# Optimization experiments

Measured on AMD Instinct MI355X. Metric: run time of the kernel, lower is better.

The kernel has to match this reference:

```python
import jax, jax.numpy as jnp
import numpy as np

DIM = 1024
NUM_HEADS = 16
HEAD_DIM = DIM // NUM_HEADS
SCALE = HEAD_DIM ** -0.5


def rotate_half(x):
    x1, x2 = jnp.split(x, 2, axis=-1)
    return jnp.concatenate((-x2, x1), axis=-1)


def setup_inputs() -> dict:
    key = jax.random.key(0)
    ks = jax.random.split(key, 8)
    B, N = 2, 2048
    x = jax.random.normal(ks[0], (B, N, DIM), dtype=jnp.float32)
    # RoPE tables, broadcast over batch and heads
    pos = jnp.arange(N, dtype=jnp.float32)[:, None]
    inv_freq = 1.0 / (10000.0 ** (jnp.arange(0, HEAD_DIM, 2, dtype=jnp.float32) / HEAD_DIM))
    ang = pos * inv_freq[None, :]                       # [N, HEAD_DIM/2]
    ang = jnp.concatenate([ang, ang], axis=-1)          # [N, HEAD_DIM]
    rope_cos = jnp.cos(ang)[None, None]                 # [1,1,N,HEAD_DIM]
    rope_sin = jnp.sin(ang)[None, None]
    s = DIM ** -0.5
    qkv_w = jax.random.normal(ks[1], (3 * DIM, DIM), dtype=jnp.float32) * s
    qkv_b = jnp.zeros((3 * DIM,), dtype=jnp.float32)
    proj_w = jax.random.normal(ks[2], (DIM, DIM), dtype=jnp.float32) * s
    proj_b = jnp.zeros((DIM,), dtype=jnp.float32)
    return {"x": x, "rope_cos": rope_cos, "rope_sin": rope_sin,
            "qkv_w": qkv_w, "qkv_b": qkv_b, "proj_w": proj_w, "proj_b": proj_b}


def reference(x, rope_cos, rope_sin, qkv_w, qkv_b, proj_w, proj_b):
    B, N, C = x.shape
    H, D = NUM_HEADS, HEAD_DIM
    qkv = x @ qkv_w.T + qkv_b                            # [B,N,3C]
    qkv = qkv.reshape(B, N, 3, H, D).transpose(2, 0, 3, 1, 4)  # [3,B,H,N,D]
    q, k, v = qkv[0], qkv[1], qkv[2]
    # RoPE on q, k
    q = q * rope_cos + rotate_half(q) * rope_sin
    k = k * rope_cos + rotate_half(k) * rope_sin
    # scaled dot-product attention
    scores = jnp.einsum('bhnd,bhmd->bhnm', q, k) * SCALE
    attn = jax.nn.softmax(scores, axis=-1)
    out = jnp.einsum('bhnm,bhmd->bhnd', attn, v)         # [B,H,N,D]
    out = out.transpose(0, 2, 1, 3).reshape(B, N, C)
    return out @ proj_w.T + proj_b
```

## Files before the change

kernel.cpp:

```cpp
#include <hip/hip_runtime.h>
#include <hip/hip_bf16.h>

#define NUM_HEADS 16
#define HEAD_DIM 64
#define DIM 1024
#define NTOK 2048
#define MTOT 4096

typedef __attribute__((ext_vector_type(8))) short bf16x8;
typedef __attribute__((ext_vector_type(4))) float f32x4;

__device__ __forceinline__ unsigned short f2bf(float f) {
    union { __hip_bfloat16 h; unsigned short u; } c;
    c.h = __float2bfloat16(f);
    return c.u;
}

__device__ __forceinline__ void gload16(const unsigned short* g, unsigned short* l) {
    __builtin_amdgcn_global_load_lds(
        (const __attribute__((address_space(1))) void*)g,
        (__attribute__((address_space(3))) void*)l, 16, 0, 0);
}

__global__ __launch_bounds__(256) void k_conv3(
    const float* __restrict__ s0, unsigned short* __restrict__ d0, int n0,
    const float* __restrict__ s1, unsigned short* __restrict__ d1, int n1,
    const float* __restrict__ s2, unsigned short* __restrict__ d2, int n2)
{
    int blk = blockIdx.x;
    int b0 = n0 >> 11, b1 = n1 >> 11;
    const float* s; unsigned short* d; int i;
    if (blk < b0)            { s = s0; d = d0; i = blk; }
    else if (blk < b0 + b1)  { s = s1; d = d1; i = blk - b0; }
    else                     { s = s2; d = d2; i = blk - b0 - b1; }
    int idx = (i * 256 + threadIdx.x) * 8;
    float4 a = *(const float4*)(s + idx);
    float4 b = *(const float4*)(s + idx + 4);
    union { unsigned short us[8]; uint4 u4; } p;
    p.us[0] = f2bf(a.x); p.us[1] = f2bf(a.y); p.us[2] = f2bf(a.z); p.us[3] = f2bf(a.w);
    p.us[4] = f2bf(b.x); p.us[5] = f2bf(b.y); p.us[6] = f2bf(b.z); p.us[7] = f2bf(b.w);
    *(uint4*)(d + idx) = p.u4;
}

__global__ __launch_bounds__(256) void k_gemm_qkv(
    const unsigned short* __restrict__ xb, const unsigned short* __restrict__ wb,
    const float* __restrict__ bias, const float* __restrict__ rcos,
    const float* __restrict__ rsin,
    unsigned short* __restrict__ qb, unsigned short* __restrict__ kb,
    unsigned short* __restrict__ vtb)
{
    __shared__ __align__(16) unsigned char smem[34816];
    unsigned short* As = (unsigned short*)smem;
    unsigned short* Bs = (unsigned short*)(smem + 16384);

    const int tid  = threadIdx.x;
    const int lane = tid & 63;
    const int wid  = tid >> 6;
    const int lr   = lane & 15;
    const int g    = lane >> 4;
    const int wm   = (wid >> 1) * 64;
    const int wn   = (wid & 1) * 64;
    const int m0   = blockIdx.x * 128;
    const int n0   = blockIdx.y * 128;

    f32x4 acc[4][4];
    #pragma unroll
    for (int i = 0; i < 4; ++i)
        #pragma unroll
        for (int j = 0; j < 4; ++j) acc[i][j] = (f32x4){0.f, 0.f, 0.f, 0.f};

    for (int k0 = 0; k0 < DIM; k0 += 64) {
        #pragma unroll
        for (int it = 0; it < 4; ++it) {
            int p   = tid + it * 256;
            int row = p >> 3;
            int c   = (p & 7) ^ (row & 7);
            gload16(xb + (size_t)(m0 + row) * DIM + k0 + c*8, As + p*8);
            gload16(wb + (size_t)(n0 + row) * DIM + k0 + c*8, Bs + p*8);
        }
        __syncthreads();
        #pragma unroll
        for (int kk = 0; kk < 2; ++kk) {
            bf16x8 af[4], bfr[4];
            #pragma unroll
            for (int i = 0; i < 4; ++i) {
                int row = wm + i*16 + lr;
                af[i] = *(const bf16x8*)(As + row*64 + (((kk*4 + g) ^ (row & 7)) << 3));
            }
            #pragma unroll
            for (int j = 0; j < 4; ++j) {
                int row = wn + j*16 + lr;
                bfr[j] = *(const bf16x8*)(Bs + row*64 + (((kk*4 + g) ^ (row & 7)) << 3));
            }
            #pragma unroll
            for (int i = 0; i < 4; ++i)
                #pragma unroll
                for (int j = 0; j < 4; ++j)
                    acc[i][j] = __builtin_amdgcn_mfma_f32_16x16x32_bf16(af[i], bfr[j], acc[i][j], 0, 0, 0);
        }
        __syncthreads();
    }

    const int sect = n0 >> 10;
    float bq[4];
    #pragma unroll
    for (int j = 0; j < 4; ++j) bq[j] = bias[n0 + wn + j*16 + lr];

    if (sect < 2) {
        unsigned short* dst = sect ? kb : qb;
        const float sc = sect ? 1.0f : 0.125f * 1.44269504088896f;
        const int h = ((n0 & 1023) + wn) >> 6;
        #pragma unroll
        for (int i = 0; i < 4; ++i) {
            #pragma unroll
            for (int v = 0; v < 4; ++v) {
                int gm = m0 + wm + i*16 + g*4 + v;
                int b  = gm >> 11, n = gm & 2047;
                size_t base = ((size_t)(b*NUM_HEADS + h) * NTOK + n) << 6;
                #pragma unroll
                for (int j = 0; j < 4; ++j) {
                    int d = j*16 + lr;
                    float val = acc[i][j][v] + bq[j];
                    float vp  = acc[i][j^2][v] + bq[j^2];
                    float rot = (j < 2) ? -vp : vp;
                    float c = rcos[n*64 + d], s = rsin[n*64 + d];
                    dst[base + d] = f2bf((val * c + rot * s) * sc);
                }
            }
        }
    } else {
        unsigned short (*vt)[136] = (unsigned short (*)[136])smem;
        __syncthreads();
        #pragma unroll
        for (int i = 0; i < 4; ++i)
            #pragma unroll
            for (int j = 0; j < 4; ++j)
                #pragma unroll
                for (int v = 0; v < 4; ++v) {
                    int row = wm + i*16 + g*4 + v;
                    int c   = wn + j*16 + lr;
                    vt[c][row] = f2bf(acc[i][j][v] + bq[j]);
                }
        __syncthreads();
        const int b = m0 >> 11;
        const int nbase = m0 & 2047;
        #pragma unroll
        for (int it = 0; it < 8; ++it) {
            int c   = (tid >> 4) + it * 16;
            int sc2 = (n0 & 1023) + c;
            int hh  = sc2 >> 6, d = sc2 & 63;
            int nloc = (tid & 15) * 8;
            uint4 val = *(uint4*)&vt[c][nloc];
            *(uint4*)(vtb + ((size_t)(b*NUM_HEADS + hh) * HEAD_DIM + d) * NTOK + nbase + nloc) = val;
        }
    }
}

__global__ __launch_bounds__(256, 4) void k_attn(
    const unsigned short* __restrict__ qb, const unsigned short* __restrict__ kb,
    const unsigned short* __restrict__ vtb, unsigned short* __restrict__ attnb)
{
    __shared__ __align__(16) char sb[40960];

    const int tid  = threadIdx.x;
    const int lane = tid & 63;
    const int w    = tid >> 6;
    const int g    = lane >> 4;
    const int lr   = lane & 15;
    const int q0   = blockIdx.x * 64;
    const int bh   = blockIdx.y;
    const int b    = bh >> 4, h = bh & 15;

    int kfoff[2][4], vfoff[2][4], paoff[2], pwoff[4][4];
    #pragma unroll
    for (int kk = 0; kk < 2; ++kk) {
        #pragma unroll
        for (int fn = 0; fn < 4; ++fn) {
            int row = fn*16 + lr;
            int sw  = ((kk*4 + g) ^ (row & 7)) << 4;
            kfoff[kk][fn] = row*128 + sw;
            vfoff[kk][fn] = 16384 + row*128 + sw;
        }
        paoff[kk] = 32768 + w*2048 + lr*128 + (((kk*4 + g) ^ (lr & 7)) << 4);
    }
    #pragma unroll
    for (int fn = 0; fn < 4; ++fn)
        #pragma unroll
        for (int v = 0; v < 4; ++v) {
            int row = g*4 + v, col = fn*16 + lr;
            pwoff[fn][v] = 32768 + w*2048 + row*128 + (((col >> 3) ^ (row & 7)) << 4) + (col & 7)*2;
        }

    const unsigned short* gk[2];
    const unsigned short* gv[2];
    char* dk[2]; char* dv[2];
    {
        const unsigned short* kbase = kb  + (size_t)bh * NTOK * 64;
        const unsigned short* vbase = vtb + (size_t)bh * HEAD_DIM * NTOK;
        #pragma unroll
        for (int hp = 0; hp < 2; ++hp) {
            int p   = tid + hp * 256;
            int row = p >> 3;
            int c   = (p & 7) ^ (row & 7);
            gk[hp] = kbase + row*64 + c*8;
            gv[hp] = vbase + (size_t)row*NTOK + c*8;
            dk[hp] = sb + p*16;
            dv[hp] = sb + 16384 + p*16;
        }
    }

    bf16x8 qa[2];
    {
        size_t qrow = ((size_t)bh * NTOK + q0 + w*16 + lr) * 64;
        #pragma unroll
        for (int kk = 0; kk < 2; ++kk)
            qa[kk] = *(const bf16x8*)(qb + qrow + kk*32 + g*8);
    }

    f32x4 o[4];
    float m_[4], lsum[4];
    #pragma unroll
    for (int fd = 0; fd < 4; ++fd) o[fd] = (f32x4){0.f, 0.f, 0.f, 0.f};
    #pragma unroll
    for (int v = 0; v < 4; ++v) { m_[v] = -1e30f; lsum[v] = 0.f; }

    #pragma unroll
    for (int hp = 0; hp < 2; ++hp) {
        gload16(gk[hp], (unsigned short*)dk[hp]);
        gload16(gv[hp], (unsigned short*)dv[hp]);
        gk[hp] += 4096; gv[hp] += 64;
    }
    __syncthreads();

#define ATTN_ITER(X, DO_STAGE)                                                   \
    {                                                                            \
        if (DO_STAGE) {                                                          \
            _Pragma("unroll")                                                    \
            for (int hp = 0; hp < 2; ++hp) {                                     \
                gload16(gk[hp], (unsigned short*)(dk[hp] + ((X) ^ 8192)));       \
                gload16(gv[hp], (unsigned short*)(dv[hp] + ((X) ^ 8192)));       \
                gk[hp] += 4096; gv[hp] += 64;                                    \
            }                                                                    \
        }                                                                        \
        f32x4 s_[4];                                                             \
        _Pragma("unroll")                                                        \
        for (int fn = 0; fn < 4; ++fn) s_[fn] = (f32x4){0.f, 0.f, 0.f, 0.f};     \
        _Pragma("unroll")                                                        \
        for (int kk = 0; kk < 2; ++kk) {                                         \
            bf16x8 kf[4];                                                        \
            _Pragma("unroll")                                                    \
            for (int fn = 0; fn < 4; ++fn)                                       \
                kf[fn] = *(const bf16x8*)(sb + kfoff[kk][fn] + (X));             \
            __builtin_amdgcn_s_setprio(1);                                       \
            _Pragma("unroll")                                                    \
            for (int fn = 0; fn < 4; ++fn)                                       \
                s_[fn] = __builtin_amdgcn_mfma_f32_16x16x32_bf16(qa[kk], kf[fn], s_[fn], 0, 0, 0); \
            __builtin_amdgcn_s_setprio(0);                                       \
        }                                                                        \
        float lmax[4]; int need = 0;                                             \
        _Pragma("unroll")                                                        \
        for (int v = 0; v < 4; ++v) {                                            \
            lmax[v] = fmaxf(fmaxf(fmaxf(s_[0][v], s_[1][v]), s_[2][v]), s_[3][v]); \
            need |= (lmax[v] > m_[v] + 8.f);                                     \
        }                                                                        \
        if (__any(need)) {                                                       \
            _Pragma("unroll")                                                    \
            for (int v = 0; v < 4; ++v) {                                        \
                float mx = lmax[v];                                              \
                mx = fmaxf(mx, __shfl_xor(mx, 1));                               \
                mx = fmaxf(mx, __shfl_xor(mx, 2));                               \
                mx = fmaxf(mx, __shfl_xor(mx, 4));                               \
                mx = fmaxf(mx, __shfl_xor(mx, 8));                               \
                float mn  = fmaxf(m_[v], mx);                                    \
                float scl = __builtin_amdgcn_exp2f(m_[v] - mn);                  \
                m_[v] = mn;                                                      \
                lsum[v] *= scl;                                                  \
                _Pragma("unroll")                                                \
                for (int fd = 0; fd < 4; ++fd) o[fd][v] *= scl;                  \
            }                                                                    \
        }                                                                        \
        _Pragma("unroll")                                                        \
        for (int fn = 0; fn < 4; ++fn)                                           \
            _Pragma("unroll")                                                    \
            for (int v = 0; v < 4; ++v) {                                        \
                float p = __builtin_amdgcn_exp2f(s_[fn][v] - m_[v]);             \
                lsum[v] += p;                                                    \
                *(unsigned short*)(sb + pwoff[fn][v]) = f2bf(p);                 \
            }                                                                    \
        _Pragma("unroll")                                                        \
        for (int kk = 0; kk < 2; ++kk) {                                         \
            bf16x8 pa = *(const bf16x8*)(sb + paoff[kk]);                        \
            bf16x8 vf[4];                                                        \
            _Pragma("unroll")                                                    \
            for (int fd = 0; fd < 4; ++fd)                                       \
                vf[fd] = *(const bf16x8*)(sb + vfoff[kk][fd] + (X));             \
            __builtin_amdgcn_s_setprio(1);                                       \
            _Pragma("unroll")                                                    \
            for (int fd = 0; fd < 4; ++fd)                                       \
                o[fd] = __builtin_amdgcn_mfma_f32_16x16x32_bf16(pa, vf[fd], o[fd], 0, 0, 0); \
            __builtin_amdgcn_s_setprio(0);                                       \
        }                                                                        \
        __syncthreads();                                                         \
    }

    #pragma unroll 1
    for (int t = 0; t < NTOK/64; t += 2) {
        ATTN_ITER(0,    true);
        ATTN_ITER(8192, (t + 2 < NTOK/64));
    }
#undef ATTN_ITER

    #pragma unroll
    for (int v = 0; v < 4; ++v) {
        float l = lsum[v];
        l += __shfl_xor(l, 1);
        l += __shfl_xor(l, 2);
        l += __shfl_xor(l, 4);
        l += __shfl_xor(l, 8);
        lsum[v] = 1.0f / l;
    }
    #pragma unroll
    for (int fd = 0; fd < 4; ++fd)
        #pragma unroll
        for (int v = 0; v < 4; ++v) {
            int n = q0 + w*16 + g*4 + v;
            attnb[((size_t)(b*NTOK + n)) * DIM + h*HEAD_DIM + fd*16 + lr] =
                f2bf(o[fd][v] * lsum[v]);
        }
}

__global__ __launch_bounds__(256) void k_proj(
    const unsigned short* __restrict__ a, const unsigned short* __restrict__ wb,
    const float* __restrict__ bias, float* __restrict__ out)
{
    __shared__ __align__(16) unsigned short As[8192];
    __shared__ __align__(16) unsigned short Bs[8192];

    const int tid  = threadIdx.x;
    const int lane = tid & 63;
    const int wid  = tid >> 6;
    const int lr   = lane & 15;
    const int g    = lane >> 4;
    const int wm   = (wid >> 1) * 64;
    const int wn   = (wid & 1) * 64;
    const int m0   = blockIdx.x * 128;
    const int n0   = blockIdx.y * 128;

    f32x4 acc[4][4];
    #pragma unroll
    for (int i = 0; i < 4; ++i)
        #pragma unroll
        for (int j = 0; j < 4; ++j) acc[i][j] = (f32x4){0.f, 0.f, 0.f, 0.f};

    for (int k0 = 0; k0 < DIM; k0 += 64) {
        #pragma unroll
        for (int it = 0; it < 4; ++it) {
            int p   = tid + it * 256;
            int row = p >> 3;
            int c   = (p & 7) ^ (row & 7);
            gload16(a  + (size_t)(m0 + row) * DIM + k0 + c*8, As + p*8);
            gload16(wb + (size_t)(n0 + row) * DIM + k0 + c*8, Bs + p*8);
        }
        __syncthreads();
        #pragma unroll
        for (int kk = 0; kk < 2; ++kk) {
            bf16x8 af[4], bfr[4];
            #pragma unroll
            for (int i = 0; i < 4; ++i) {
                int row = wm + i*16 + lr;
                af[i] = *(const bf16x8*)(As + row*64 + (((kk*4 + g) ^ (row & 7)) << 3));
            }
            #pragma unroll
            for (int j = 0; j < 4; ++j) {
                int row = wn + j*16 + lr;
                bfr[j] = *(const bf16x8*)(Bs + row*64 + (((kk*4 + g) ^ (row & 7)) << 3));
            }
            #pragma unroll
            for (int i = 0; i < 4; ++i)
                #pragma unroll
                for (int j = 0; j < 4; ++j)
                    acc[i][j] = __builtin_amdgcn_mfma_f32_16x16x32_bf16(af[i], bfr[j], acc[i][j], 0, 0, 0);
        }
        __syncthreads();
    }

    #pragma unroll
    for (int i = 0; i < 4; ++i)
        #pragma unroll
        for (int j = 0; j < 4; ++j)
            #pragma unroll
            for (int v = 0; v < 4; ++v) {
                int row = m0 + wm + i*16 + g*4 + v;
                int col = n0 + wn + j*16 + lr;
                out[(size_t)row * DIM + col] = acc[i][j][v] + bias[col];
            }
}

extern "C" void kernel_launch(void* const* d_in, const int* in_sizes, int n_in,
                              void* d_out, int out_size, void* d_ws, size_t ws_size,
                              hipStream_t stream)
{
    const float* x      = (const float*)d_in[0];
    const float* rcos   = (const float*)d_in[1];
    const float* rsin   = (const float*)d_in[2];
    const float* qkv_w  = (const float*)d_in[3];
    const float* qkv_b  = (const float*)d_in[4];
    const float* proj_w = (const float*)d_in[5];
    const float* proj_b = (const float*)d_in[6];
    float* out = (float*)d_out;

    const size_t BUF = (size_t)2 * NUM_HEADS * NTOK * HEAD_DIM;
    unsigned short* qb    = (unsigned short*)d_ws;
    unsigned short* kb    = qb + BUF;
    unsigned short* vtb   = kb + BUF;
    unsigned short* attnb = vtb + BUF;
    unsigned short* xbf   = attnb + BUF;
    unsigned short* wqkvb = xbf + (size_t)MTOT * DIM;
    unsigned short* wprjb = wqkvb + (size_t)3 * DIM * DIM;

    const int n0 = MTOT * DIM, n1 = 3 * DIM * DIM, n2 = DIM * DIM;
    k_conv3<<<dim3((n0 + n1 + n2) / 2048), 256, 0, stream>>>(
        x, xbf, n0, qkv_w, wqkvb, n1, proj_w, wprjb, n2);

    k_gemm_qkv<<<dim3(32, 24), 256, 0, stream>>>(xbf, wqkvb, qkv_b, rcos, rsin, qb, kb, vtb);
    k_attn<<<dim3(NTOK/64, 32), 256, 0, stream>>>(qb, kb, vtb, attnb);
    k_proj<<<dim3(32, 8), 256, 0, stream>>>(attnb, wprjb, proj_b, out);
}
```

Before: 135.7 us.

## Transpose attention MFMA layout so each lane owns one query row

Swaps the MFMA operand order so S and O are computed transposed, which gives each lane a single query row. Row max then needs only two cross-lane shuffles instead of four per row, and P is written as packed 8-byte stores instead of scalar 2-byte stores. The row sum is now taken by an extra MFMA against a ones vector, so it uses bf16-rounded P rather than fp32 sums. Output is written as packed 8-byte stores.

Result: faster. 127.9 us (-5.8%).

```diff
diff --git a/kernel.cpp b/kernel.cpp
--- a/kernel.cpp
+++ b/kernel.cpp
@@ -171,9 +171,9 @@
     const int bh   = blockIdx.y;
     const int b    = bh >> 4, h = bh & 15;
 
-    int kfoff[2][4], vfoff[2][4], paoff[2], pwoff[4][4];
-    #pragma unroll
-    for (int kk = 0; kk < 2; ++kk) {
+    int kfoff[2][4], vfoff[2][4];
+    #pragma unroll
+    for (int kk = 0; kk < 2; ++kk)
         #pragma unroll
         for (int fn = 0; fn < 4; ++fn) {
             int row = fn*16 + lr;
@@ -181,15 +181,14 @@
             kfoff[kk][fn] = row*128 + sw;
             vfoff[kk][fn] = 16384 + row*128 + sw;
         }
-        paoff[kk] = 32768 + w*2048 + lr*128 + (((kk*4 + g) ^ (lr & 7)) << 4);
-    }
+    const int pswz = (lr & 7) << 1;
+    int pwoff[4], proff[2];
     #pragma unroll
     for (int fn = 0; fn < 4; ++fn)
-        #pragma unroll
-        for (int v = 0; v < 4; ++v) {
-            int row = g*4 + v, col = fn*16 + lr;
-            pwoff[fn][v] = 32768 + w*2048 + row*128 + (((col >> 3) ^ (row & 7)) << 4) + (col & 7)*2;
-        }
+        pwoff[fn] = 32768 + w*2048 + lr*128 + (((fn*4 + g) ^ pswz) << 3);
+    #pragma unroll
+    for (int kk = 0; kk < 2; ++kk)
+        proff[kk] = 32768 + w*2048 + lr*128 + (((kk*8 + g*2) ^ pswz) << 3);
 
     const unsigned short* gk[2];
     const unsigned short* gv[2];
@@ -217,12 +216,16 @@
             qa[kk] = *(const bf16x8*)(qb + qrow + kk*32 + g*8);
     }
 
-    f32x4 o[4];
-    float m_[4], lsum[4];
-    #pragma unroll
-    for (int fd = 0; fd < 4; ++fd) o[fd] = (f32x4){0.f, 0.f, 0.f, 0.f};
-    #pragma unroll
-    for (int v = 0; v < 4; ++v) { m_[v] = -1e30f; lsum[v] = 0.f; }
+    const f32x4 z4 = {0.f, 0.f, 0.f, 0.f};
+    bf16x8 onesa;
+    #pragma unroll
+    for (int j = 0; j < 8; ++j) onesa[j] = (short)0x3F80;
+
+    f32x4 o2[4];
+    f32x4 ol = z4;
+    float m_ = -1e30f;
+    #pragma unroll
+    for (int fd = 0; fd < 4; ++fd) o2[fd] = z4;
 
     #pragma unroll
     for (int hp = 0; hp < 2; ++hp) {
@@ -243,61 +246,56 @@
             }                                                                    \
         }                                                                        \
         f32x4 s_[4];                                                             \
+        __builtin_amdgcn_s_setprio(1);                                           \
         _Pragma("unroll")                                                        \
-        for (int fn = 0; fn < 4; ++fn) s_[fn] = (f32x4){0.f, 0.f, 0.f, 0.f};     \
+        for (int fn = 0; fn < 4; ++fn) {                                         \
+            bf16x8 kf = *(const bf16x8*)(sb + kfoff[0][fn] + (X));               \
+            s_[fn] = __builtin_amdgcn_mfma_f32_16x16x32_bf16(kf, qa[0], z4, 0, 0, 0); \
+        }                                                                        \
+        _Pragma("unroll")                                                        \
+        for (int fn = 0; fn < 4; ++fn) {                                         \
+            bf16x8 kf = *(const bf16x8*)(sb + kfoff[1][fn] + (X));               \
+            s_[fn] = __builtin_amdgcn_mfma_f32_16x16x32_bf16(kf, qa[1], s_[fn], 0, 0, 0); \
+        }                                                                        \
+        __builtin_amdgcn_s_setprio(0);                                           \
+        float mmA = fmaxf(fmaxf(s_[0][0], s_[0][1]), fmaxf(s_[0][2], s_[0][3])); \
+        float mmB = fmaxf(fmaxf(s_[1][0], s_[1][1]), fmaxf(s_[1][2], s_[1][3])); \
+        float mmC = fmaxf(fmaxf(s_[2][0], s_[2][1]), fmaxf(s_[2][2], s_[2][3])); \
+        float mmD = fmaxf(fmaxf(s_[3][0], s_[3][1]), fmaxf(s_[3][2], s_[3][3])); \
+        float lmax = fmaxf(fmaxf(mmA, mmB), fmaxf(mmC, mmD));                    \
+        if (__any(lmax > m_ + 8.f)) {                                            \
+            float mx = fmaxf(lmax, __shfl_xor(lmax, 16));                        \
+            mx = fmaxf(mx, __shfl_xor(mx, 32));                                  \
+            float mn  = fmaxf(m_, mx);                                           \
+            float scl = __builtin_amdgcn_exp2f(m_ - mn);                         \
+            m_ = mn;                                                             \
+            _Pragma("unroll")                                                    \
+            for (int v = 0; v < 4; ++v) ol[v] *= scl;                            \
+            _Pragma("unroll")                                                    \
+            for (int fd = 0; fd < 4; ++fd)                                       \
+                _Pragma("unroll")                                                \
+                for (int v = 0; v < 4; ++v) o2[fd][v] *= scl;                    \
+        }                                                                        \
+        _Pragma("unroll")                                                        \
+        for (int fn = 0; fn < 4; ++fn) {                                         \
+            union { unsigned short us[4]; uint2 u2; } pk4;                       \
+            _Pragma("unroll")                                                    \
+            for (int v = 0; v < 4; ++v)                                          \
+                pk4.us[v] = f2bf(__builtin_amdgcn_exp2f(s_[fn][v] - m_));        \
+            *(uint2*)(sb + pwoff[fn]) = pk4.u2;                                  \
+        }                                                                        \
         _Pragma("unroll")                                                        \
         for (int kk = 0; kk < 2; ++kk) {                                         \
-            bf16x8 kf[4];                                                        \
-            _Pragma("unroll")                                                    \
-            for (int fn = 0; fn < 4; ++fn)                                       \
-                kf[fn] = *(const bf16x8*)(sb + kfoff[kk][fn] + (X));             \
-            __builtin_amdgcn_s_setprio(1);                                       \
-            _Pragma("unroll")                                                    \
-            for (int fn = 0; fn < 4; ++fn)                                       \
-                s_[fn] = __builtin_amdgcn_mfma_f32_16x16x32_bf16(qa[kk], kf[fn], s_[fn], 0, 0, 0); \
-            __builtin_amdgcn_s_setprio(0);                                       \
-        }                                                                        \
-        float lmax[4]; int need = 0;                                             \
-        _Pragma("unroll")                                                        \
-        for (int v = 0; v < 4; ++v) {                                            \
-            lmax[v] = fmaxf(fmaxf(fmaxf(s_[0][v], s_[1][v]), s_[2][v]), s_[3][v]); \
-            need |= (lmax[v] > m_[v] + 8.f);                                     \
-        }                                                                        \
-        if (__any(need)) {                                                       \
-            _Pragma("unroll")                                                    \
-            for (int v = 0; v < 4; ++v) {                                        \
-                float mx = lmax[v];                                              \
-                mx = fmaxf(mx, __shfl_xor(mx, 1));                               \
-                mx = fmaxf(mx, __shfl_xor(mx, 2));                               \
-                mx = fmaxf(mx, __shfl_xor(mx, 4));                               \
-                mx = fmaxf(mx, __shfl_xor(mx, 8));                               \
-                float mn  = fmaxf(m_[v], mx);                                    \
-                float scl = __builtin_amdgcn_exp2f(m_[v] - mn);                  \
-                m_[v] = mn;                                                      \
-                lsum[v] *= scl;                                                  \
-                _Pragma("unroll")                                                \
-                for (int fd = 0; fd < 4; ++fd) o[fd][v] *= scl;                  \
-            }                                                                    \
-        }                                                                        \
-        _Pragma("unroll")                                                        \
-        for (int fn = 0; fn < 4; ++fn)                                           \
-            _Pragma("unroll")                                                    \
-            for (int v = 0; v < 4; ++v) {                                        \
-                float p = __builtin_amdgcn_exp2f(s_[fn][v] - m_[v]);             \
-                lsum[v] += p;                                                    \
-                *(unsigned short*)(sb + pwoff[fn][v]) = f2bf(p);                 \
-            }                                                                    \
-        _Pragma("unroll")                                                        \
-        for (int kk = 0; kk < 2; ++kk) {                                         \
-            bf16x8 pa = *(const bf16x8*)(sb + paoff[kk]);                        \
+            bf16x8 pb = *(const bf16x8*)(sb + proff[kk]);                        \
             bf16x8 vf[4];                                                        \
             _Pragma("unroll")                                                    \
             for (int fd = 0; fd < 4; ++fd)                                       \
                 vf[fd] = *(const bf16x8*)(sb + vfoff[kk][fd] + (X));             \
             __builtin_amdgcn_s_setprio(1);                                       \
+            ol = __builtin_amdgcn_mfma_f32_16x16x32_bf16(onesa, pb, ol, 0, 0, 0); \
             _Pragma("unroll")                                                    \
             for (int fd = 0; fd < 4; ++fd)                                       \
-                o[fd] = __builtin_amdgcn_mfma_f32_16x16x32_bf16(pa, vf[fd], o[fd], 0, 0, 0); \
+                o2[fd] = __builtin_amdgcn_mfma_f32_16x16x32_bf16(vf[fd], pb, o2[fd], 0, 0, 0); \
             __builtin_amdgcn_s_setprio(0);                                       \
         }                                                                        \
         __syncthreads();                                                         \
@@ -310,23 +308,15 @@
     }
 #undef ATTN_ITER
 
-    #pragma unroll
-    for (int v = 0; v < 4; ++v) {
-        float l = lsum[v];
-        l += __shfl_xor(l, 1);
-        l += __shfl_xor(l, 2);
-        l += __shfl_xor(l, 4);
-        l += __shfl_xor(l, 8);
-        lsum[v] = 1.0f / l;
-    }
-    #pragma unroll
-    for (int fd = 0; fd < 4; ++fd)
-        #pragma unroll
-        for (int v = 0; v < 4; ++v) {
-            int n = q0 + w*16 + g*4 + v;
-            attnb[((size_t)(b*NTOK + n)) * DIM + h*HEAD_DIM + fd*16 + lr] =
-                f2bf(o[fd][v] * lsum[v]);
-        }
+    const float inv = 1.0f / ol[0];
+    const size_t obase = ((size_t)(b*NTOK + q0 + w*16 + lr)) * DIM + h*HEAD_DIM + g*4;
+    #pragma unroll
+    for (int fd = 0; fd < 4; ++fd) {
+        union { unsigned short us[4]; uint2 u2; } pk4;
+        #pragma unroll
+        for (int v = 0; v < 4; ++v) pk4.us[v] = f2bf(o2[fd][v] * inv);
+        *(uint2*)(attnb + obase + fd*16) = pk4.u2;
+    }
 }
 
 __global__ __launch_bounds__(256) void k_proj(
```
